# Performance work log

Measured on AMD Instinct MI355X. Metric: run time of the kernel, lower is better.

Reference implementation:

```python
import jax, jax.numpy as jnp
import numpy as np

RF = 3          # receptive_field_size (cubic)
STRIDE = 1
TEMP = 1.0      # softmax temperature ('soft' sampling, eval mode: no Gumbel noise)
TREE_DEPTH = 4

# Truth table of all 16 binary gates: GATES[g, t] = value of gate g on input
# pattern t = 2*a + b (a = first child, b = second child), t in {0,1,2,3}.
GATES = np.array([[(g >> t) & 1 for t in range(4)] for g in range(16)],
                 dtype=np.float32)  # (16, 4)


def _lut_eval(a, b, w):
    """Differentiable 2-input LUT. a, b: (B,K,P,nodes); w: (nodes,K,16)."""
    probs = jax.nn.softmax(w / TEMP, axis=-1)          # (nodes,K,16)
    lut = probs @ jnp.asarray(GATES)                   # (nodes,K,4) relaxed truth table
    lut = jnp.moveaxis(lut, 0, 1)[:, None]             # (K,1,nodes,4) -> bcast over B,P
    l0, l1, l2, l3 = lut[..., 0], lut[..., 1], lut[..., 2], lut[..., 3]
    na, nb = 1.0 - a, 1.0 - b
    # E[lut(a,b)] under independent Bernoulli inputs
    return l0 * na * nb + l1 * na * b + l2 * a * nb + l3 * a * b


def setup_inputs() -> dict:
    key = jax.random.key(0)
    ks = jax.random.split(key, 8)
    B, C, H, W, D = 4, 3, 32, 32, 32
    K, S = 32, 16  # num_kernels, lut_rank**tree_depth leaves
    x = jax.random.uniform(ks[0], (B, C, H, W, D), dtype=jnp.float32)
    # (lut_rank=2, K, S, 4) coords (h, w, d, c); rf=3 and channels=3 so all in [0,3)
    kernel_coords = jax.random.randint(ks[1], (2, K, S, 4), 0, 3, dtype=jnp.int32)
    w0 = jax.random.normal(ks[2], (16, K, 16), dtype=jnp.float32)
    w1 = jax.random.normal(ks[3], (8, K, 16), dtype=jnp.float32)
    w2 = jax.random.normal(ks[4], (4, K, 16), dtype=jnp.float32)
    w3 = jax.random.normal(ks[5], (2, K, 16), dtype=jnp.float32)
    w4 = jax.random.normal(ks[6], (1, K, 16), dtype=jnp.float32)
    return {"x": x, "kernel_coords": kernel_coords,
            "w0": w0, "w1": w1, "w2": w2, "w3": w3, "w4": w4}


def reference(x, kernel_coords, w0, w1, w2, w3, w4):
    B, C, H, W, D = x.shape
    OH, OW, OD = (H - RF) // STRIDE + 1, (W - RF) // STRIDE + 1, (D - RF) // STRIDE + 1
    kc = kernel_coords
    # linear offset of each leaf coord inside flattened (C,H,W,D) volume
    base = ((kc[..., 3] * H + kc[..., 0]) * W + kc[..., 1]) * D + kc[..., 2]  # (2,K,S)
    oh = jnp.arange(OH) * STRIDE
    ow = jnp.arange(OW) * STRIDE
    od = jnp.arange(OD) * STRIDE
    patch = ((oh[:, None, None] * W + ow[None, :, None]) * D
             + od[None, None, :]).reshape(-1)                                  # (P,)
    lin = base[:, :, None, :] + patch[None, None, :, None]                     # (2,K,P,S)
    g = x.reshape(B, -1)[:, lin]                                               # (B,2,K,P,S)
    out = _lut_eval(g[:, 0], g[:, 1], w0)                                      # (B,K,P,S)
    for w in (w1, w2, w3, w4):  # binary tree reduction over TREE_DEPTH levels
        out = _lut_eval(out[..., 0::2], out[..., 1::2], w)
    return out.reshape(B, out.shape[1], OH, OW, OD)
```

## Files before the change

kernel.cpp:

```cpp
#include <hip/hip_runtime.h>


#define B_  4
#define C_  3
#define H_  32
#define W_  32
#define D_  32
#define K_  32
#define S_  16
#define WS  33
#define TPB 256

typedef float v8f __attribute__((ext_vector_type(8), aligned(4)));

__device__ __forceinline__ v8f lut8(v8f a, v8f b, float l0, float d1, float d2, float d3) {
    const v8f t0 = a * d2 + l0;
    const v8f t1 = a * d3 + d1;
    return b * t1 + t0;
}

__global__ __launch_bounds__(TPB, 3) void logic_conv3d(
    const float* __restrict__ x,
    const int*   __restrict__ kc,
    const float* __restrict__ w0,
    const float* __restrict__ w1,
    const float* __restrict__ w2,
    const float* __restrict__ w3,
    const float* __restrict__ w4,
    float*       __restrict__ out)
{
    __shared__ float4 s_lut[31];
    __shared__ int    s_lb[32];
    __shared__ __align__(16) float slab[12 * 32 * WS];

    const int bk  = blockIdx.x;
    const int b   = bk >> 5;
    const int k   = bk & 31;
    const int tid = threadIdx.x;

    if (tid < 31) {
        const float* wp; int ln;
        if      (tid < 16) { wp = w0; ln = tid;      }
        else if (tid < 24) { wp = w1; ln = tid - 16; }
        else if (tid < 28) { wp = w2; ln = tid - 24; }
        else if (tid < 30) { wp = w3; ln = tid - 28; }
        else               { wp = w4; ln = 0;        }
        const float* wrow = wp + (ln * K_ + k) * 16;
        float lg[16];
        float m = -1e30f;
        #pragma unroll
        for (int g = 0; g < 16; ++g) { lg[g] = wrow[g]; m = fmaxf(m, lg[g]); }
        float z = 0.f;
        #pragma unroll
        for (int g = 0; g < 16; ++g) { lg[g] = __expf(lg[g] - m); z += lg[g]; }
        const float inv = 1.0f / z;
        float l0 = 0.f, l1 = 0.f, l2 = 0.f, l3 = 0.f;
        #pragma unroll
        for (int g = 0; g < 16; ++g) {
            float p = lg[g] * inv;
            if (g & 1) l0 += p;
            if (g & 2) l1 += p;
            if (g & 4) l2 += p;
            if (g & 8) l3 += p;
        }
        s_lut[tid] = make_float4(l0, l1 - l0, l2 - l0, (l3 - l2) - (l1 - l0));
    } else if (tid >= 32 && tid < 64) {
        const int idx  = tid - 32;
        const int tree = idx >> 4;
        const int s    = idx & 15;
        const int off  = ((tree * K_ + k) * S_ + s) * 4;
        const int h = kc[off + 0], w = kc[off + 1], d = kc[off + 2], c = kc[off + 3];
        s_lb[idx] = ((c * 4 + h) * 32 + w) * WS + d;
    }

    {
        const float* xb = x + (size_t)b * (C_ * H_ * W_ * D_) + (blockIdx.y * 2) * (W_ * D_);
        const int w  = tid >> 3;
        const int d4 = (tid & 7) << 2;
        #pragma unroll
        for (int it = 0; it < 12; ++it) {
            const int c  = it >> 2;
            const int dh = it & 3;
            const float4 val = *(const float4*)(xb + c * (H_ * W_ * D_) + dh * (W_ * D_) + tid * 4);
            *(float4*)&slab[((c * 4 + dh) * 32 + w) * WS + d4] = val;
        }
    }
    __syncthreads();

    int sAB[32];
    #pragma unroll
    for (int i = 0; i < 8; ++i) {
        const int4 q = *(const int4*)&s_lb[i * 4];
        sAB[i * 4 + 0] = __builtin_amdgcn_readfirstlane(q.x);
        sAB[i * 4 + 1] = __builtin_amdgcn_readfirstlane(q.y);
        sAB[i * 4 + 2] = __builtin_amdgcn_readfirstlane(q.z);
        sAB[i * 4 + 3] = __builtin_amdgcn_readfirstlane(q.w);
    }

    const int ohl = tid >> 7;
    const int r   = tid & 127;
    const int ow  = r >> 2;
    const int gq  = r & 3;
    const int od0 = (gq < 3) ? (gq << 3) : 22;

    if (ow < 30) {
        const int vo = ohl * (32 * WS) + ow * WS + od0;

        v8f v1[8];
        #pragma unroll
        for (int j = 0; j < 8; ++j) {
            const int s0 = 2 * j, s1 = 2 * j + 1;
            const v8f A0 = *(const v8f*)&slab[sAB[s0] + vo];
            const v8f B0 = *(const v8f*)&slab[sAB[16 + s0] + vo];
            const float4 L0 = s_lut[s0];
            const v8f t0 = lut8(A0, B0, L0.x, L0.y, L0.z, L0.w);
            const v8f A1 = *(const v8f*)&slab[sAB[s1] + vo];
            const v8f B1 = *(const v8f*)&slab[sAB[16 + s1] + vo];
            const float4 L1 = s_lut[s1];
            const v8f t1 = lut8(A1, B1, L1.x, L1.y, L1.z, L1.w);
            const float4 LN = s_lut[16 + j];
            v1[j] = lut8(t0, t1, LN.x, LN.y, LN.z, LN.w);
        }

        #pragma unroll
        for (int j = 0; j < 4; ++j) {
            const float4 L = s_lut[24 + j];
            v1[j] = lut8(v1[2 * j], v1[2 * j + 1], L.x, L.y, L.z, L.w);
        }
        #pragma unroll
        for (int j = 0; j < 2; ++j) {
            const float4 L = s_lut[28 + j];
            v1[j] = lut8(v1[2 * j], v1[2 * j + 1], L.x, L.y, L.z, L.w);
        }
        {
            const float4 L = s_lut[30];
            v1[0] = lut8(v1[0], v1[1], L.x, L.y, L.z, L.w);
        }

        const int oh = blockIdx.y * 2 + ohl;
        float* outp = out + (size_t)bk * 27000 + oh * 900 + ow * 30 + od0;
        *(v8f*)outp = v1[0];
    }
}

extern "C" void kernel_launch(void* const* d_in, const int* in_sizes, int n_in,
                              void* d_out, int out_size, void* d_ws, size_t ws_size,
                              hipStream_t stream) {
    const float* x  = (const float*)d_in[0];
    const int*   kc = (const int*)d_in[1];
    const float* w0 = (const float*)d_in[2];
    const float* w1 = (const float*)d_in[3];
    const float* w2 = (const float*)d_in[4];
    const float* w3 = (const float*)d_in[5];
    const float* w4 = (const float*)d_in[6];
    float* out = (float*)d_out;

    dim3 grid(B_ * K_, 15);
    logic_conv3d<<<grid, TPB, 0, stream>>>(x, kc, w0, w1, w2, w3, w4, out);
}
```

Baseline: 87.49 us.

## Replace LDS slab staging with fp16 d-shifted global copies read directly

Adds a prepass kernel that converts x to fp16 and writes three copies shifted by 0, 1 and 2 along d, so every leaf read becomes an aligned 16-byte vector load straight from global memory. The shared-memory slab fill and its bank-padding layout are removed, and occupancy is raised to 4 blocks per SM. The goal is to drop the per-block LDS staging and cut the bytes read per gather. The cost is an extra kernel launch, fp16 rounding of the inputs, and gathers that now depend on cache hits instead of LDS.

```diff
diff --git a/kernel.cpp b/kernel.cpp
--- a/kernel.cpp
+++ b/kernel.cpp
@@ -8,10 +8,20 @@
 #define D_  32
 #define K_  32
 #define S_  16
-#define WS  33
 #define TPB 256
+#define NX  393216
 
-typedef float v8f __attribute__((ext_vector_type(8), aligned(4)));
+typedef float    v8f __attribute__((ext_vector_type(8)));
+typedef _Float16 h8  __attribute__((ext_vector_type(8), aligned(16)));
+typedef float    f4a __attribute__((ext_vector_type(4), aligned(4)));
+typedef float    f2a __attribute__((ext_vector_type(2), aligned(4)));
+
+__device__ __forceinline__ v8f cvt8(h8 h) {
+    v8f r;
+    #pragma unroll
+    for (int i = 0; i < 8; ++i) r[i] = (float)h[i];
+    return r;
+}
 
 __device__ __forceinline__ v8f lut8(v8f a, v8f b, float l0, float d1, float d2, float d3) {
     const v8f t0 = a * d2 + l0;
@@ -19,19 +29,30 @@
     return b * t1 + t0;
 }
 
-__global__ __launch_bounds__(TPB, 3) void logic_conv3d(
-    const float* __restrict__ x,
-    const int*   __restrict__ kc,
-    const float* __restrict__ w0,
-    const float* __restrict__ w1,
-    const float* __restrict__ w2,
-    const float* __restrict__ w3,
-    const float* __restrict__ w4,
-    float*       __restrict__ out)
+__global__ __launch_bounds__(TPB) void prepass(const float* __restrict__ x,
+                                               _Float16* __restrict__ y) {
+    const int i = blockIdx.x * TPB + threadIdx.x;
+    const int d = i & 31;
+    const float v0 = x[i];
+    const float v1 = (d < 31) ? x[i + 1] : 0.f;
+    const float v2 = (d < 30) ? x[i + 2] : 0.f;
+    y[i]          = (_Float16)v0;
+    y[NX + i]     = (_Float16)v1;
+    y[2 * NX + i] = (_Float16)v2;
+}
+
+__global__ __launch_bounds__(TPB, 4) void logic_conv3d(
+    const _Float16* __restrict__ y,
+    const int*      __restrict__ kc,
+    const float*    __restrict__ w0,
+    const float*    __restrict__ w1,
+    const float*    __restrict__ w2,
+    const float*    __restrict__ w3,
+    const float*    __restrict__ w4,
+    float*          __restrict__ out)
 {
     __shared__ float4 s_lut[31];
     __shared__ int    s_lb[32];
-    __shared__ __align__(16) float slab[12 * 32 * WS];
 
     const int bk  = blockIdx.x;
     const int b   = bk >> 5;
@@ -70,20 +91,7 @@
         const int s    = idx & 15;
         const int off  = ((tree * K_ + k) * S_ + s) * 4;
         const int h = kc[off + 0], w = kc[off + 1], d = kc[off + 2], c = kc[off + 3];
-        s_lb[idx] = ((c * 4 + h) * 32 + w) * WS + d;
-    }
-
-    {
-        const float* xb = x + (size_t)b * (C_ * H_ * W_ * D_) + (blockIdx.y * 2) * (W_ * D_);
-        const int w  = tid >> 3;
-        const int d4 = (tid & 7) << 2;
-        #pragma unroll
-        for (int it = 0; it < 12; ++it) {
-            const int c  = it >> 2;
-            const int dh = it & 3;
-            const float4 val = *(const float4*)(xb + c * (H_ * W_ * D_) + dh * (W_ * D_) + tid * 4);
-            *(float4*)&slab[((c * 4 + dh) * 32 + w) * WS + d4] = val;
-        }
+        s_lb[idx] = d * NX + ((c * H_ + h) * W_ + w) * D_;
     }
     __syncthreads();
 
@@ -101,21 +109,22 @@
     const int r   = tid & 127;
     const int ow  = r >> 2;
     const int gq  = r & 3;
-    const int od0 = (gq < 3) ? (gq << 3) : 22;
+    const int od0 = gq << 3;
 
     if (ow < 30) {
-        const int vo = ohl * (32 * WS) + ow * WS + od0;
+        const int oh   = blockIdx.y * 2 + ohl;
+        const int voff = b * (C_ * H_ * W_ * D_) + oh * (W_ * D_) + ow * D_ + od0;
 
         v8f v1[8];
         #pragma unroll
         for (int j = 0; j < 8; ++j) {
             const int s0 = 2 * j, s1 = 2 * j + 1;
-            const v8f A0 = *(const v8f*)&slab[sAB[s0] + vo];
-            const v8f B0 = *(const v8f*)&slab[sAB[16 + s0] + vo];
+            const v8f A0 = cvt8(*(const h8*)(y + sAB[s0]      + voff));
+            const v8f B0 = cvt8(*(const h8*)(y + sAB[16 + s0] + voff));
             const float4 L0 = s_lut[s0];
             const v8f t0 = lut8(A0, B0, L0.x, L0.y, L0.z, L0.w);
-            const v8f A1 = *(const v8f*)&slab[sAB[s1] + vo];
-            const v8f B1 = *(const v8f*)&slab[sAB[16 + s1] + vo];
+            const v8f A1 = cvt8(*(const h8*)(y + sAB[s1]      + voff));
+            const v8f B1 = cvt8(*(const h8*)(y + sAB[16 + s1] + voff));
             const float4 L1 = s_lut[s1];
             const v8f t1 = lut8(A1, B1, L1.x, L1.y, L1.z, L1.w);
             const float4 LN = s_lut[16 + j];
@@ -137,9 +146,16 @@
             v1[0] = lut8(v1[0], v1[1], L.x, L.y, L.z, L.w);
         }
 
-        const int oh = blockIdx.y * 2 + ohl;
         float* outp = out + (size_t)bk * 27000 + oh * 900 + ow * 30 + od0;
-        *(v8f*)outp = v1[0];
+        f4a lo; lo[0] = v1[0][0]; lo[1] = v1[0][1]; lo[2] = v1[0][2]; lo[3] = v1[0][3];
+        *(f4a*)outp = lo;
+        if (gq < 3) {
+            f4a hi; hi[0] = v1[0][4]; hi[1] = v1[0][5]; hi[2] = v1[0][6]; hi[3] = v1[0][7];
+            *(f4a*)(outp + 4) = hi;
+        } else {
+            f2a hi2; hi2[0] = v1[0][4]; hi2[1] = v1[0][5];
+            *(f2a*)(outp + 4) = hi2;
+        }
     }
 }
 
@@ -154,7 +170,9 @@
     const float* w3 = (const float*)d_in[5];
     const float* w4 = (const float*)d_in[6];
     float* out = (float*)d_out;
+    _Float16* y = (_Float16*)d_ws;
 
+    prepass<<<NX / TPB, TPB, 0, stream>>>(x, y);
     dim3 grid(B_ * K_, 15);
-    logic_conv3d<<<grid, TPB, 0, stream>>>(x, kc, w0, w1, w2, w3, w4, out);
+    logic_conv3d<<<grid, TPB, 0, stream>>>(y, kc, w0, w1, w2, w3, w4, out);
 }
```

Measured after the change: 86.44 us. About the same (-1.2%).
